# Kernel optimization log

Hardware: AMD Instinct MI355X
Metric: run time of the kernel (lower is better)

Reference implementation:

```python
import jax, jax.numpy as jnp
import numpy as np

CTX = 2048
D_IN = 1024
D_OUT = 1024
BATCH = 8


def setup_inputs() -> dict:
    key = jax.random.key(0)
    k1, k2, k3, k4 = jax.random.split(key, 4)
    x = jax.random.normal(k1, (BATCH, CTX, D_IN), dtype=jnp.float32)
    # nn.Linear weight is [out, in]; store pre-transposed as [in, out] for x @ W
    Wk = jax.random.normal(k2, (D_IN, D_OUT), dtype=jnp.float32) * (1.0 / np.sqrt(D_IN))
    Wq = jax.random.normal(k3, (D_IN, D_OUT), dtype=jnp.float32) * (1.0 / np.sqrt(D_IN))
    Wv = jax.random.normal(k4, (D_IN, D_OUT), dtype=jnp.float32) * (1.0 / np.sqrt(D_IN))
    return {"x": x, "Wq": Wq, "Wk": Wk, "Wv": Wv}


def reference(x, Wq, Wk, Wv):
    # projections: [b, s, d_out]
    q = jnp.einsum('bsi,io->bso', x, Wq)
    k = jnp.einsum('bsi,io->bso', x, Wk)
    v = jnp.einsum('bsi,io->bso', x, Wv)
    s = q.shape[1]
    scale = 1.0 / jnp.sqrt(jnp.asarray(q.shape[-1], q.dtype))
    att = jnp.einsum('bqd,bkd->bqk', q, k) * scale  # [b, s, s]
    # additive causal mask: 0 on/below diagonal, -inf above
    causal = jnp.tril(jnp.ones((s, s), dtype=bool))
    att = jnp.where(causal, att, -jnp.inf)
    att = jax.nn.softmax(att, axis=-1)
    return jnp.einsum('bqk,bkd->bqd', att, v)
```

## Files before the change

### kernel.cpp

```cpp
#include <hip/hip_runtime.h>
#include <stdint.h>

typedef unsigned short u16;
typedef short bf16x8 __attribute__((ext_vector_type(8)));
typedef float f32x4 __attribute__((ext_vector_type(4)));

#define CTX 2048
#define DIN 1024
#define DOUT 1024
#define NB 8

__device__ __forceinline__ u16 f2bf(float f) {
  uint32_t u = __builtin_bit_cast(uint32_t, f);
  u += 0x7FFFu + ((u >> 16) & 1u);
  return (u16)(u >> 16);
}

__device__ __forceinline__ void gld_lds16(const u16* g, const u16* lds) {
  __builtin_amdgcn_global_load_lds(
      (const __attribute__((address_space(1))) uint32_t*)(unsigned long long)(const void*)g,
      (__attribute__((address_space(3))) uint32_t*)(uint32_t)(unsigned long long)(const void*)lds,
      16, 0, 0);
}

#define SBAR() asm volatile("s_barrier" ::: "memory")
#define VMCNT4() asm volatile("s_waitcnt vmcnt(4)" ::: "memory")
#define VMCNT0() asm volatile("s_waitcnt vmcnt(0)" ::: "memory")
#define SCHED0() __builtin_amdgcn_sched_barrier(0)

template <typename EPI>
__device__ __forceinline__ void gemm256(const u16* __restrict__ A, int lda,
                                        const u16* __restrict__ Bt, int ldb,
                                        int m0, int n0, int K, EPI&& epi) {
  __shared__ __align__(16) u16 lds[65536];

  const int t = threadIdx.x;
  const int lane = t & 63;
  const int w = t >> 6;
  const int wm = w >> 2;
  const int wn = w & 3;
  const int l15 = lane & 15;
  const int l16 = lane >> 4;
  const int nkt = K >> 6;
  const int bf0 = (wn & 1) * 4;

  f32x4 acc[8][4];
#pragma unroll
  for (int i = 0; i < 8; ++i)
#pragma unroll
    for (int j = 0; j < 4; ++j) acc[i][j] = {0.f, 0.f, 0.f, 0.f};

  const u16* gA0 = A + (size_t)(m0 + w * 16 + l15) * lda + l16 * 8;
  const u16* gA1 = gA0 + (size_t)128 * lda;
  const u16* gB0 = Bt + (size_t)(n0 + w * 16 + l15) * ldb + l16 * 8;
  const u16* gB1 = gB0 + (size_t)128 * ldb;

  auto STAGEH = [&](int bb, int rr, const u16* g) {
    u16* d = lds + (((bb * 4 + rr) * 16) + w * 2) * 512;
    gld_lds16(g, d);
    gld_lds16(g + 32, d + 512);
  };

  STAGEH(0, 0, gA0);
  STAGEH(0, 1, gA1);
  STAGEH(0, 2, gB0);
  STAGEH(0, 3, gB1);
  if (nkt > 1) {
    STAGEH(1, 0, gA0 + 64);
    STAGEH(1, 1, gA1 + 64);
  }
  VMCNT4();
  SBAR();

  bf16x8 ar[8][2], br[2][2];

  for (int T = 0; T < nkt; ++T) {
    const int b = T & 1;
    const u16* bufA = lds + ((b * 4 + wm) * 16) * 512 + lane * 8;
    const u16* bufB = lds + ((b * 4 + 2 + (wn >> 1)) * 16) * 512 + lane * 8;

#pragma unroll
    for (int fr = 0; fr < 4; ++fr)
#pragma unroll
      for (int ks = 0; ks < 2; ++ks)
        ar[fr][ks] = *reinterpret_cast<const bf16x8*>(bufA + (fr * 2 + ks) * 512);
#pragma unroll
    for (int nc = 0; nc < 2; ++nc)
#pragma unroll
      for (int ks = 0; ks < 2; ++ks)
        br[nc][ks] = *reinterpret_cast<const bf16x8*>(bufB + ((bf0 + nc) * 2 + ks) * 512);
    if (T + 1 < nkt) STAGEH(b ^ 1, 2, gB0 + (size_t)(T + 1) * 64);
    SBAR();
    SCHED0();
    __builtin_amdgcn_s_setprio(1);
#pragma unroll
    for (int fr = 0; fr < 4; ++fr)
#pragma unroll
      for (int nc = 0; nc < 2; ++nc)
#pragma unroll
        for (int ks = 0; ks < 2; ++ks)
          acc[fr][nc] = __builtin_amdgcn_mfma_f32_16x16x32_bf16(ar[fr][ks], br[nc][ks],
                                                                acc[fr][nc], 0, 0, 0);
    __builtin_amdgcn_s_setprio(0);
    SCHED0();
    SBAR();

#pragma unroll
    for (int fr = 4; fr < 8; ++fr)
#pragma unroll
      for (int ks = 0; ks < 2; ++ks)
        ar[fr][ks] = *reinterpret_cast<const bf16x8*>(bufA + (fr * 2 + ks) * 512);
    if (T + 1 < nkt) STAGEH(b ^ 1, 3, gB1 + (size_t)(T + 1) * 64);
    SBAR();
    SCHED0();
    __builtin_amdgcn_s_setprio(1);
#pragma unroll
    for (int fr = 4; fr < 8; ++fr)
#pragma unroll
      for (int nc = 0; nc < 2; ++nc)
#pragma unroll
        for (int ks = 0; ks < 2; ++ks)
          acc[fr][nc] = __builtin_amdgcn_mfma_f32_16x16x32_bf16(ar[fr][ks], br[nc][ks],
                                                                acc[fr][nc], 0, 0, 0);
    __builtin_amdgcn_s_setprio(0);
    SCHED0();
    SBAR();

#pragma unroll
    for (int nc = 0; nc < 2; ++nc)
#pragma unroll
      for (int ks = 0; ks < 2; ++ks)
        br[nc][ks] = *reinterpret_cast<const bf16x8*>(bufB + ((bf0 + 2 + nc) * 2 + ks) * 512);
    if (T + 2 < nkt) STAGEH(b, 0, gA0 + (size_t)(T + 2) * 64);
    SBAR();
    SCHED0();
    __builtin_amdgcn_s_setprio(1);
#pragma unroll
    for (int fr = 0; fr < 4; ++fr)
#pragma unroll
      for (int nc = 0; nc < 2; ++nc)
#pragma unroll
        for (int ks = 0; ks < 2; ++ks)
          acc[fr][2 + nc] = __builtin_amdgcn_mfma_f32_16x16x32_bf16(ar[fr][ks], br[nc][ks],
                                                                    acc[fr][2 + nc], 0, 0, 0);
    __builtin_amdgcn_s_setprio(0);
    SCHED0();
    SBAR();

    if (T + 2 < nkt) STAGEH(b, 1, gA1 + (size_t)(T + 2) * 64);
    SBAR();
    SCHED0();
    __builtin_amdgcn_s_setprio(1);
#pragma unroll
    for (int fr = 4; fr < 8; ++fr)
#pragma unroll
      for (int nc = 0; nc < 2; ++nc)
#pragma unroll
        for (int ks = 0; ks < 2; ++ks)
          acc[fr][2 + nc] = __builtin_amdgcn_mfma_f32_16x16x32_bf16(ar[fr][ks], br[nc][ks],
                                                                    acc[fr][2 + nc], 0, 0, 0);
    __builtin_amdgcn_s_setprio(0);
    SCHED0();
    if (T + 2 < nkt) {
      VMCNT4();
    } else {
      VMCNT0();
    }
    SBAR();
  }

  epi(acc, wm * 128 + l16 * 4, wn * 64 + l15);
}

__global__ __launch_bounds__(256) void k_cvt_x(const float* __restrict__ x,
                                               u16* __restrict__ xb) {
  const int idx = (blockIdx.x * 256 + threadIdx.x) * 4;
  const float4 v = *reinterpret_cast<const float4*>(x + idx);
  ushort4 o;
  o.x = f2bf(v.x); o.y = f2bf(v.y); o.z = f2bf(v.z); o.w = f2bf(v.w);
  *reinterpret_cast<ushort4*>(xb + idx) = o;
}

__global__ __launch_bounds__(256) void k_cvt_wt(const float* __restrict__ W,
                                                u16* __restrict__ Wt) {
  __shared__ u16 tile[64][65];
  const int bc = blockIdx.x;
  const int tr0 = (bc >> 4) * 64;
  const int tc0 = (bc & 15) * 64;
  const int t = threadIdx.x;
  const int col = t & 63, rr = t >> 6;
#pragma unroll
  for (int p = 0; p < 16; ++p) {
    const int row = rr * 16 + p;
    tile[row][col] = f2bf(W[(size_t)(tr0 + row) * DOUT + tc0 + col]);
  }
  __syncthreads();
#pragma unroll
  for (int p = 0; p < 16; ++p) {
    const int row = rr * 16 + p;
    Wt[(size_t)(tc0 + row) * DIN + tr0 + col] = tile[col][row];
  }
}

__global__ __launch_bounds__(512, 2) void k_proj(const u16* __restrict__ xb,
                                                 const u16* __restrict__ Wt,
                                                 u16* __restrict__ qkb,
                                                 u16* __restrict__ vT) {
  const int wg = (blockIdx.x & 7) * 96 + (blockIdx.x >> 3);
  const int m0 = (wg / 12) * 256, n0 = (wg % 12) * 256;
  gemm256(xb, DIN, Wt, DIN, m0, n0, DIN,
          [&](const f32x4(&acc)[8][4], int r0, int c0) {
            if (n0 < 2 * DOUT) {
#pragma unroll
              for (int fr = 0; fr < 8; ++fr)
#pragma unroll
                for (int nc = 0; nc < 4; ++nc) {
                  const int r = m0 + r0 + fr * 16;
                  const int c = n0 + c0 + nc * 16;
#pragma unroll
                  for (int i = 0; i < 4; ++i)
                    qkb[(size_t)(r + i) * 2048 + c] = f2bf(acc[fr][nc][i]);
                }
            } else {
              const int b = m0 >> 11;
              const int sl = (m0 & (CTX - 1)) + r0;
              u16* C = vT + (size_t)b * DOUT * CTX;
#pragma unroll
              for (int fr = 0; fr < 8; ++fr)
#pragma unroll
                for (int nc = 0; nc < 4; ++nc) {
                  const int d = n0 - 2 * DOUT + c0 + nc * 16;
                  const int s = sl + fr * 16;
                  ushort4 o;
                  o.x = f2bf(acc[fr][nc][0]);
                  o.y = f2bf(acc[fr][nc][1]);
                  o.z = f2bf(acc[fr][nc][2]);
                  o.w = f2bf(acc[fr][nc][3]);
                  *reinterpret_cast<ushort4*>(C + (size_t)d * CTX + s) = o;
                }
            }
          });
}

__global__ __launch_bounds__(512, 2) void k_score(const u16* __restrict__ qkb,
                                                  float* __restrict__ S) {
  const int u = (blockIdx.x & 7) * 36 + (blockIdx.x >> 3);
  const int b = u / 36, v = u % 36;
  int it = 0;
  while ((it + 1) * (it + 2) / 2 <= v) ++it;
  const int jt = v - it * (it + 1) / 2;
  const u16* Aq = qkb + (size_t)b * CTX * 2048;
  float* C = S + ((size_t)b << 22);
  const int m0 = it * 256, n0 = jt * 256;
  gemm256(Aq, 2048, Aq + 1024, 2048, m0, n0, DOUT,
          [&](const f32x4(&acc)[8][4], int r0, int c0) {
#pragma unroll
            for (int fr = 0; fr < 8; ++fr)
#pragma unroll
              for (int nc = 0; nc < 4; ++nc) {
                const int r = m0 + r0 + fr * 16;
                const int c = n0 + c0 + nc * 16;
#pragma unroll
                for (int i = 0; i < 4; ++i)
                  C[(size_t)(r + i) * CTX + c] = acc[fr][nc][i] * 0.03125f;
              }
          });
}

__global__ __launch_bounds__(256) void k_softmax(float* __restrict__ Sws) {
  const int row = blockIdx.x;
  const int b = row >> 11, i = row & (CTX - 1);
  const float* srow = Sws + ((size_t)b << 22) + ((size_t)i << 11);
  u16* prow = (u16*)(Sws + ((size_t)b << 22)) + ((size_t)i << 12);
  const int t = threadIdx.x;
  const int j0 = t * 8;
  float vv[8];
  if (j0 <= i) {
    const float4 v0 = *reinterpret_cast<const float4*>(srow + j0);
    const float4 v1 = *reinterpret_cast<const float4*>(srow + j0 + 4);
    vv[0] = v0.x; vv[1] = v0.y; vv[2] = v0.z; vv[3] = v0.w;
    vv[4] = v1.x; vv[5] = v1.y; vv[6] = v1.z; vv[7] = v1.w;
  } else {
#pragma unroll
    for (int p = 0; p < 8; ++p) vv[p] = -3.0e38f;
  }
  float mx = -3.0e38f;
#pragma unroll
  for (int p = 0; p < 8; ++p) {
    vv[p] = (j0 + p <= i) ? vv[p] : -3.0e38f;
    mx = fmaxf(mx, vv[p]);
  }
#pragma unroll
  for (int off = 32; off > 0; off >>= 1) mx = fmaxf(mx, __shfl_xor(mx, off));
  __shared__ float redm[4], reds[4];
  const int lane = t & 63, wid = t >> 6;
  if (lane == 0) redm[wid] = mx;
  __syncthreads();
  mx = fmaxf(fmaxf(redm[0], redm[1]), fmaxf(redm[2], redm[3]));
  float e[8], s = 0.f;
#pragma unroll
  for (int p = 0; p < 8; ++p) {
    e[p] = __expf(vv[p] - mx);
    s += e[p];
  }
#pragma unroll
  for (int off = 32; off > 0; off >>= 1) s += __shfl_xor(s, off);
  if (lane == 0) reds[wid] = s;
  __syncthreads();
  s = reds[0] + reds[1] + reds[2] + reds[3];
  const float inv = 1.0f / s;
  ushort4 o0, o1;
  o0.x = (j0 + 0 <= i) ? f2bf(e[0] * inv) : (u16)0;
  o0.y = (j0 + 1 <= i) ? f2bf(e[1] * inv) : (u16)0;
  o0.z = (j0 + 2 <= i) ? f2bf(e[2] * inv) : (u16)0;
  o0.w = (j0 + 3 <= i) ? f2bf(e[3] * inv) : (u16)0;
  o1.x = (j0 + 4 <= i) ? f2bf(e[4] * inv) : (u16)0;
  o1.y = (j0 + 5 <= i) ? f2bf(e[5] * inv) : (u16)0;
  o1.z = (j0 + 6 <= i) ? f2bf(e[6] * inv) : (u16)0;
  o1.w = (j0 + 7 <= i) ? f2bf(e[7] * inv) : (u16)0;
  *reinterpret_cast<ushort4*>(prow + j0) = o0;
  *reinterpret_cast<ushort4*>(prow + j0 + 4) = o1;
}

__global__ __launch_bounds__(512, 2) void k_out(const float* __restrict__ Sws,
                                                const u16* __restrict__ vT,
                                                float* __restrict__ out) {
  const int idx = blockIdx.x;
  const int it = 7 - (idx >> 5);
  const int b = (idx >> 2) & 7;
  const int nt = idx & 3;
  const u16* P = (const u16*)(Sws + ((size_t)b << 22));
  const u16* Bt = vT + (size_t)b * DOUT * CTX;
  float* C = out + (size_t)b * CTX * DOUT;
  const int m0 = it * 256, n0 = nt * 256;
  gemm256(P, 2 * CTX, Bt, CTX, m0, n0, (it + 1) * 256,
          [&](const f32x4(&acc)[8][4], int r0, int c0) {
#pragma unroll
            for (int fr = 0; fr < 8; ++fr)
#pragma unroll
              for (int nc = 0; nc < 4; ++nc) {
                const int r = m0 + r0 + fr * 16;
                const int c = n0 + c0 + nc * 16;
#pragma unroll
                for (int i = 0; i < 4; ++i)
                  C[(size_t)(r + i) * DOUT + c] = acc[fr][nc][i];
              }
          });
}

extern "C" void kernel_launch(void* const* d_in, const int* in_sizes, int n_in,
                              void* d_out, int out_size, void* d_ws, size_t ws_size,
                              hipStream_t stream) {
  (void)in_sizes; (void)n_in; (void)out_size; (void)ws_size;
  const float* x = (const float*)d_in[0];
  const float* Wq = (const float*)d_in[1];
  const float* Wk = (const float*)d_in[2];
  const float* Wv = (const float*)d_in[3];
  float* out = (float*)d_out;
  uint8_t* ws = (uint8_t*)d_ws;

  float* S = (float*)ws;
  u16* xb = (u16*)ws;
  u16* Wt_all = (u16*)(ws + 33554432ull);
  u16* qkb = (u16*)(ws + 134217728ull);
  u16* vT = (u16*)(ws + 201326592ull);

  k_cvt_x<<<16384, 256, 0, stream>>>(x, xb);
  k_cvt_wt<<<256, 256, 0, stream>>>(Wq, Wt_all);
  k_cvt_wt<<<256, 256, 0, stream>>>(Wk, Wt_all + 1024ull * 1024);
  k_cvt_wt<<<256, 256, 0, stream>>>(Wv, Wt_all + 2048ull * 1024);
  k_proj<<<768, 512, 0, stream>>>(xb, Wt_all, qkb, vT);
  k_score<<<288, 512, 0, stream>>>(qkb, S);
  k_softmax<<<NB * CTX, 256, 0, stream>>>(S);
  k_out<<<256, 512, 0, stream>>>(S, vT, out);
}
```

Baseline: 330.1 us.

## Software-pipeline LDS fragment loads behind MFMA phases in GEMM main loop

Restructures the 4-phase GEMM main loop so each phase's LDS register loads for the next phase are issued right after the current MFMA block. A and B fragments for the next k-tile are prefetched at the end of the iteration, with a prologue added before the loop. It also reorders the MFMA quadrants and global-to-LDS staging, and removes several barriers per iteration so LDS latency is hidden behind matrix math. This costs extra VGPRs for the split A fragment arrays and needs care about buffer-reuse hazards.

```diff
diff --git a/kernel.cpp b/kernel.cpp
--- a/kernel.cpp
+++ b/kernel.cpp
@@ -72,25 +72,33 @@
   VMCNT4();
   SBAR();
 
-  bf16x8 ar[8][2], br[2][2];
+  bf16x8 arLo[4][2], arHi[4][2], br[2][2];
+
+  {
+    if (1 < nkt) STAGEH(1, 2, gB0 + 64);
+    const u16* bufA = lds + ((0 * 4 + wm) * 16) * 512 + lane * 8;
+    const u16* bufB = lds + ((0 * 4 + 2 + (wn >> 1)) * 16) * 512 + lane * 8;
+#pragma unroll
+    for (int fr = 0; fr < 4; ++fr)
+#pragma unroll
+      for (int ks = 0; ks < 2; ++ks)
+        arLo[fr][ks] = *reinterpret_cast<const bf16x8*>(bufA + (fr * 2 + ks) * 512);
+#pragma unroll
+    for (int nc = 0; nc < 2; ++nc)
+#pragma unroll
+      for (int ks = 0; ks < 2; ++ks)
+        br[nc][ks] = *reinterpret_cast<const bf16x8*>(bufB + ((bf0 + nc) * 2 + ks) * 512);
+    SBAR();
+  }
 
   for (int T = 0; T < nkt; ++T) {
     const int b = T & 1;
     const u16* bufA = lds + ((b * 4 + wm) * 16) * 512 + lane * 8;
     const u16* bufB = lds + ((b * 4 + 2 + (wn >> 1)) * 16) * 512 + lane * 8;
-
-#pragma unroll
-    for (int fr = 0; fr < 4; ++fr)
-#pragma unroll
-      for (int ks = 0; ks < 2; ++ks)
-        ar[fr][ks] = *reinterpret_cast<const bf16x8*>(bufA + (fr * 2 + ks) * 512);
-#pragma unroll
-    for (int nc = 0; nc < 2; ++nc)
-#pragma unroll
-      for (int ks = 0; ks < 2; ++ks)
-        br[nc][ks] = *reinterpret_cast<const bf16x8*>(bufB + ((bf0 + nc) * 2 + ks) * 512);
-    if (T + 1 < nkt) STAGEH(b ^ 1, 2, gB0 + (size_t)(T + 1) * 64);
-    SBAR();
+    const u16* bufAn = lds + (((b ^ 1) * 4 + wm) * 16) * 512 + lane * 8;
+    const u16* bufBn = lds + (((b ^ 1) * 4 + 2 + (wn >> 1)) * 16) * 512 + lane * 8;
+
+    if (T + 1 < nkt) STAGEH(b ^ 1, 3, gB1 + (size_t)(T + 1) * 64);
     SCHED0();
     __builtin_amdgcn_s_setprio(1);
 #pragma unroll
@@ -99,40 +107,38 @@
       for (int nc = 0; nc < 2; ++nc)
 #pragma unroll
         for (int ks = 0; ks < 2; ++ks)
-          acc[fr][nc] = __builtin_amdgcn_mfma_f32_16x16x32_bf16(ar[fr][ks], br[nc][ks],
+          acc[fr][nc] = __builtin_amdgcn_mfma_f32_16x16x32_bf16(arLo[fr][ks], br[nc][ks],
                                                                 acc[fr][nc], 0, 0, 0);
     __builtin_amdgcn_s_setprio(0);
     SCHED0();
-    SBAR();
-
-#pragma unroll
-    for (int fr = 4; fr < 8; ++fr)
+#pragma unroll
+    for (int fr = 0; fr < 4; ++fr)
 #pragma unroll
       for (int ks = 0; ks < 2; ++ks)
-        ar[fr][ks] = *reinterpret_cast<const bf16x8*>(bufA + (fr * 2 + ks) * 512);
-    if (T + 1 < nkt) STAGEH(b ^ 1, 3, gB1 + (size_t)(T + 1) * 64);
-    SBAR();
+        arHi[fr][ks] = *reinterpret_cast<const bf16x8*>(bufA + ((fr + 4) * 2 + ks) * 512);
+    SBAR();
+
+    if (T + 2 < nkt) STAGEH(b, 0, gA0 + (size_t)(T + 2) * 64);
     SCHED0();
     __builtin_amdgcn_s_setprio(1);
 #pragma unroll
-    for (int fr = 4; fr < 8; ++fr)
-#pragma unroll
-      for (int nc = 0; nc < 2; ++nc)
-#pragma unroll
-        for (int ks = 0; ks < 2; ++ks)
-          acc[fr][nc] = __builtin_amdgcn_mfma_f32_16x16x32_bf16(ar[fr][ks], br[nc][ks],
-                                                                acc[fr][nc], 0, 0, 0);
+    for (int fr = 0; fr < 4; ++fr)
+#pragma unroll
+      for (int nc = 0; nc < 2; ++nc)
+#pragma unroll
+        for (int ks = 0; ks < 2; ++ks)
+          acc[4 + fr][nc] = __builtin_amdgcn_mfma_f32_16x16x32_bf16(arHi[fr][ks], br[nc][ks],
+                                                                    acc[4 + fr][nc], 0, 0, 0);
     __builtin_amdgcn_s_setprio(0);
     SCHED0();
-    SBAR();
-
 #pragma unroll
     for (int nc = 0; nc < 2; ++nc)
 #pragma unroll
       for (int ks = 0; ks < 2; ++ks)
         br[nc][ks] = *reinterpret_cast<const bf16x8*>(bufB + ((bf0 + 2 + nc) * 2 + ks) * 512);
-    if (T + 2 < nkt) STAGEH(b, 0, gA0 + (size_t)(T + 2) * 64);
-    SBAR();
+    SBAR();
+
+    if (T + 2 < nkt) STAGEH(b, 1, gA1 + (size_t)(T + 2) * 64);
     SCHED0();
     __builtin_amdgcn_s_setprio(1);
 #pragma unroll
@@ -141,30 +147,41 @@
       for (int nc = 0; nc < 2; ++nc)
 #pragma unroll
         for (int ks = 0; ks < 2; ++ks)
-          acc[fr][2 + nc] = __builtin_amdgcn_mfma_f32_16x16x32_bf16(ar[fr][ks], br[nc][ks],
-                                                                    acc[fr][2 + nc], 0, 0, 0);
-    __builtin_amdgcn_s_setprio(0);
-    SCHED0();
-    SBAR();
-
-    if (T + 2 < nkt) STAGEH(b, 1, gA1 + (size_t)(T + 2) * 64);
-    SBAR();
-    SCHED0();
-    __builtin_amdgcn_s_setprio(1);
-#pragma unroll
-    for (int fr = 4; fr < 8; ++fr)
-#pragma unroll
-      for (int nc = 0; nc < 2; ++nc)
-#pragma unroll
-        for (int ks = 0; ks < 2; ++ks)
-          acc[fr][2 + nc] = __builtin_amdgcn_mfma_f32_16x16x32_bf16(ar[fr][ks], br[nc][ks],
-                                                                    acc[fr][2 + nc], 0, 0, 0);
+          acc[4 + fr][2 + nc] = __builtin_amdgcn_mfma_f32_16x16x32_bf16(arHi[fr][ks], br[nc][ks],
+                                                                        acc[4 + fr][2 + nc], 0, 0, 0);
     __builtin_amdgcn_s_setprio(0);
     SCHED0();
     if (T + 2 < nkt) {
       VMCNT4();
     } else {
       VMCNT0();
+    }
+    SBAR();
+
+    if (T + 2 < nkt) STAGEH(b, 2, gB0 + (size_t)(T + 2) * 64);
+    SCHED0();
+    __builtin_amdgcn_s_setprio(1);
+#pragma unroll
+    for (int fr = 0; fr < 4; ++fr)
+#pragma unroll
+      for (int nc = 0; nc < 2; ++nc)
+#pragma unroll
+        for (int ks = 0; ks < 2; ++ks)
+          acc[fr][2 + nc] = __builtin_amdgcn_mfma_f32_16x16x32_bf16(arLo[fr][ks], br[nc][ks],
+                                                                    acc[fr][2 + nc], 0, 0, 0);
+    __builtin_amdgcn_s_setprio(0);
+    SCHED0();
+    if (T + 1 < nkt) {
+#pragma unroll
+      for (int fr = 0; fr < 4; ++fr)
+#pragma unroll
+        for (int ks = 0; ks < 2; ++ks)
+          arLo[fr][ks] = *reinterpret_cast<const bf16x8*>(bufAn + (fr * 2 + ks) * 512);
+#pragma unroll
+      for (int nc = 0; nc < 2; ++nc)
+#pragma unroll
+        for (int ks = 0; ks < 2; ++ks)
+          br[nc][ks] = *reinterpret_cast<const bf16x8*>(bufBn + ((bf0 + nc) * 2 + ks) * 512);
     }
     SBAR();
   }
```

New measurement: 312.4 us. 1.06x faster.

## Restructure GEMM mainloop to triple-buffered K=32 tiles with single sync per step

Applied to the files above, without the earlier changes.

Replaces the double-buffered K=64 mainloop, which had four phases each with its own barriers and staged half-tiles, with a triple-buffered ring of K=32 tiles. Each iteration issues the prefetch for tile T+2 up front, loads all A/B fragments, runs one block of 32 MFMAs, and ends with a single barrier. This cuts the number of barriers per K element and simplifies scheduling, and it shrinks the LDS footprint (48K instead of 64K u16 elements). In exchange each iteration does less MFMA work per barrier and per wait, which may expose more load latency.

```diff
diff --git a/kernel.cpp b/kernel.cpp
--- a/kernel.cpp
+++ b/kernel.cpp
@@ -32,7 +32,7 @@
 __device__ __forceinline__ void gemm256(const u16* __restrict__ A, int lda,
                                         const u16* __restrict__ Bt, int ldb,
                                         int m0, int n0, int K, EPI&& epi) {
-  __shared__ __align__(16) u16 lds[65536];
+  __shared__ __align__(16) u16 lds[49152];
 
   const int t = threadIdx.x;
   const int lane = t & 63;
@@ -41,8 +41,7 @@
   const int wn = w & 3;
   const int l15 = lane & 15;
   const int l16 = lane >> 4;
-  const int nkt = K >> 6;
-  const int bf0 = (wn & 1) * 4;
+  const int nkt = K >> 5;
 
   f32x4 acc[8][4];
 #pragma unroll
@@ -50,115 +49,47 @@
 #pragma unroll
     for (int j = 0; j < 4; ++j) acc[i][j] = {0.f, 0.f, 0.f, 0.f};
 
-  const u16* gA0 = A + (size_t)(m0 + w * 16 + l15) * lda + l16 * 8;
-  const u16* gA1 = gA0 + (size_t)128 * lda;
-  const u16* gB0 = Bt + (size_t)(n0 + w * 16 + l15) * ldb + l16 * 8;
-  const u16* gB1 = gB0 + (size_t)128 * ldb;
-
-  auto STAGEH = [&](int bb, int rr, const u16* g) {
-    u16* d = lds + (((bb * 4 + rr) * 16) + w * 2) * 512;
-    gld_lds16(g, d);
-    gld_lds16(g + 32, d + 512);
+  const u16* gA = A + (size_t)(m0 + w * 16 + l15) * lda + l16 * 8;
+  const u16* gB = Bt + (size_t)(n0 + w * 16 + l15) * ldb + l16 * 8;
+  const size_t ldJA = (size_t)128 * lda;
+  const size_t ldJB = (size_t)128 * ldb;
+
+  auto STAGE = [&](int kbuf, int T) {
+    const size_t koff = (size_t)T * 32;
+    u16* base = lds + kbuf * 16384;
+    gld_lds16(gA + koff, base + w * 512);
+    gld_lds16(gA + koff + ldJA, base + 4096 + w * 512);
+    gld_lds16(gB + koff, base + 8192 + w * 512);
+    gld_lds16(gB + koff + ldJB, base + 12288 + w * 512);
   };
 
-  STAGEH(0, 0, gA0);
-  STAGEH(0, 1, gA1);
-  STAGEH(0, 2, gB0);
-  STAGEH(0, 3, gB1);
-  if (nkt > 1) {
-    STAGEH(1, 0, gA0 + 64);
-    STAGEH(1, 1, gA1 + 64);
-  }
+  STAGE(0, 0);
+  STAGE(1, 1);
   VMCNT4();
   SBAR();
 
-  bf16x8 ar[8][2], br[2][2];
-
+  int cb = 0;
+  int sb = 2;
   for (int T = 0; T < nkt; ++T) {
-    const int b = T & 1;
-    const u16* bufA = lds + ((b * 4 + wm) * 16) * 512 + lane * 8;
-    const u16* bufB = lds + ((b * 4 + 2 + (wn >> 1)) * 16) * 512 + lane * 8;
-
-#pragma unroll
-    for (int fr = 0; fr < 4; ++fr)
-#pragma unroll
-      for (int ks = 0; ks < 2; ++ks)
-        ar[fr][ks] = *reinterpret_cast<const bf16x8*>(bufA + (fr * 2 + ks) * 512);
-#pragma unroll
-    for (int nc = 0; nc < 2; ++nc)
-#pragma unroll
-      for (int ks = 0; ks < 2; ++ks)
-        br[nc][ks] = *reinterpret_cast<const bf16x8*>(bufB + ((bf0 + nc) * 2 + ks) * 512);
-    if (T + 1 < nkt) STAGEH(b ^ 1, 2, gB0 + (size_t)(T + 1) * 64);
-    SBAR();
-    SCHED0();
+    if (T + 2 < nkt) STAGE(sb, T + 2);
+
+    const u16* bufA = lds + cb * 16384 + (wm * 8) * 512 + lane * 8;
+    const u16* bufB = lds + cb * 16384 + 8192 + (wn * 4) * 512 + lane * 8;
+    bf16x8 ar[8], br[4];
+#pragma unroll
+    for (int fr = 0; fr < 8; ++fr)
+      ar[fr] = *reinterpret_cast<const bf16x8*>(bufA + fr * 512);
+#pragma unroll
+    for (int nc = 0; nc < 4; ++nc)
+      br[nc] = *reinterpret_cast<const bf16x8*>(bufB + nc * 512);
+
     __builtin_amdgcn_s_setprio(1);
 #pragma unroll
-    for (int fr = 0; fr < 4; ++fr)
-#pragma unroll
-      for (int nc = 0; nc < 2; ++nc)
-#pragma unroll
-        for (int ks = 0; ks < 2; ++ks)
-          acc[fr][nc] = __builtin_amdgcn_mfma_f32_16x16x32_bf16(ar[fr][ks], br[nc][ks],
-                                                                acc[fr][nc], 0, 0, 0);
-    __builtin_amdgcn_s_setprio(0);
-    SCHED0();
-    SBAR();
-
-#pragma unroll
-    for (int fr = 4; fr < 8; ++fr)
-#pragma unroll
-      for (int ks = 0; ks < 2; ++ks)
-        ar[fr][ks] = *reinterpret_cast<const bf16x8*>(bufA + (fr * 2 + ks) * 512);
-    if (T + 1 < nkt) STAGEH(b ^ 1, 3, gB1 + (size_t)(T + 1) * 64);
-    SBAR();
-    SCHED0();
-    __builtin_amdgcn_s_setprio(1);
-#pragma unroll
-    for (int fr = 4; fr < 8; ++fr)
-#pragma unroll
-      for (int nc = 0; nc < 2; ++nc)
-#pragma unroll
-        for (int ks = 0; ks < 2; ++ks)
-          acc[fr][nc] = __builtin_amdgcn_mfma_f32_16x16x32_bf16(ar[fr][ks], br[nc][ks],
-                                                                acc[fr][nc], 0, 0, 0);
-    __builtin_amdgcn_s_setprio(0);
-    SCHED0();
-    SBAR();
-
-#pragma unroll
-    for (int nc = 0; nc < 2; ++nc)
-#pragma unroll
-      for (int ks = 0; ks < 2; ++ks)
-        br[nc][ks] = *reinterpret_cast<const bf16x8*>(bufB + ((bf0 + 2 + nc) * 2 + ks) * 512);
-    if (T + 2 < nkt) STAGEH(b, 0, gA0 + (size_t)(T + 2) * 64);
-    SBAR();
-    SCHED0();
-    __builtin_amdgcn_s_setprio(1);
-#pragma unroll
-    for (int fr = 0; fr < 4; ++fr)
-#pragma unroll
-      for (int nc = 0; nc < 2; ++nc)
-#pragma unroll
-        for (int ks = 0; ks < 2; ++ks)
-          acc[fr][2 + nc] = __builtin_amdgcn_mfma_f32_16x16x32_bf16(ar[fr][ks], br[nc][ks],
-                                                                    acc[fr][2 + nc], 0, 0, 0);
-    __builtin_amdgcn_s_setprio(0);
-    SCHED0();
-    SBAR();
-
-    if (T + 2 < nkt) STAGEH(b, 1, gA1 + (size_t)(T + 2) * 64);
-    SBAR();
-    SCHED0();
-    __builtin_amdgcn_s_setprio(1);
-#pragma unroll
-    for (int fr = 4; fr < 8; ++fr)
-#pragma unroll
-      for (int nc = 0; nc < 2; ++nc)
-#pragma unroll
-        for (int ks = 0; ks < 2; ++ks)
-          acc[fr][2 + nc] = __builtin_amdgcn_mfma_f32_16x16x32_bf16(ar[fr][ks], br[nc][ks],
-                                                                    acc[fr][2 + nc], 0, 0, 0);
+    for (int fr = 0; fr < 8; ++fr)
+#pragma unroll
+      for (int nc = 0; nc < 4; ++nc)
+        acc[fr][nc] = __builtin_amdgcn_mfma_f32_16x16x32_bf16(ar[fr], br[nc],
+                                                              acc[fr][nc], 0, 0, 0);
     __builtin_amdgcn_s_setprio(0);
     SCHED0();
     if (T + 2 < nkt) {
@@ -167,6 +98,8 @@
       VMCNT0();
     }
     SBAR();
+    cb = (cb == 2) ? 0 : cb + 1;
+    sb = (sb == 2) ? 0 : sb + 1;
   }
 
   epi(acc, wm * 128 + l16 * 4, wn * 64 + l15);
```

Measured after the change: 320.2 us. 3.0% less time.
